# Kernel tuning notes

Hardware: AMD Instinct MI355X
Metric: run time of the kernel (lower is better)

The kernel has to match this reference:

```python
import jax, jax.numpy as jnp
import numpy as np

L = 10      # LSTM layers
H = 128     # hidden size
ENC = 4096  # traffic_encoder_output_len
B = 8192    # batch
T = 12      # points_to_predict
NUM_MODES = 25


def setup_inputs() -> dict:
    key = jax.random.key(0)
    ks = jax.random.split(key, 10)
    s = 1.0 / np.sqrt(H)
    return {
        "backbone_encoded": jax.random.normal(ks[0], (B, ENC), jnp.float32),
        "fc_in_W": jax.random.normal(ks[1], (H, ENC), jnp.float32) / np.sqrt(ENC),
        "fc_in_b": jax.random.normal(ks[2], (H,), jnp.float32) * s,
        "Wih": jax.random.normal(ks[3], (L, 4 * H, H), jnp.float32) * s,
        "Whh": jax.random.normal(ks[4], (L, 4 * H, H), jnp.float32) * s,
        "bih": jax.random.normal(ks[5], (L, 4 * H), jnp.float32) * s,
        "bhh": jax.random.normal(ks[6], (L, 4 * H), jnp.float32) * s,
        "fc_out_W": jax.random.normal(ks[7], (3 * NUM_MODES, H), jnp.float32) * s,
        "fc_out_b": jax.random.normal(ks[8], (3 * NUM_MODES,), jnp.float32) * s,
        "points_to_predict": T,
    }


def _lstm_stack(x, Wih, Whh, bih, bhh):
    # x: [B, T, H]; PyTorch gate order: i, f, g, o
    def run_layer(x, l):
        def step(carry, xt):
            h, c = carry
            gates = xt @ Wih[l].T + h @ Whh[l].T + bih[l] + bhh[l]  # [B, 4H]
            i, f, g, o = jnp.split(gates, 4, axis=-1)
            c = jax.nn.sigmoid(f) * c + jax.nn.sigmoid(i) * jnp.tanh(g)
            h = jax.nn.sigmoid(o) * jnp.tanh(c)
            return (h, c), h
        b = x.shape[0]
        h0 = jnp.zeros((b, H), x.dtype)
        _, ys = jax.lax.scan(step, (h0, h0), jnp.swapaxes(x, 0, 1))  # [T, B, H]
        return jnp.swapaxes(ys, 0, 1)

    for l in range(L):
        x = run_layer(x, l)
    return x


def reference(backbone_encoded, fc_in_W, fc_in_b, Wih, Whh, bih, bhh,
              fc_out_W, fc_out_b, points_to_predict):
    enc = jax.nn.relu(backbone_encoded @ fc_in_W.T + fc_in_b)        # [B, H]
    x = jnp.repeat(enc[:, None, :], points_to_predict, axis=1)      # [B, T, H]
    y = _lstm_stack(x, Wih, Whh, bih, bhh)                           # [B, T, H]
    fc = y @ fc_out_W.T + fc_out_b                                   # [B, T, 75]
    b, t, _ = fc.shape
    # chunk(25, dim=channels) of consecutive pairs -> [B, 25, T, 2]
    predictions = fc[:, :, :50].reshape(b, t, NUM_MODES, 2).transpose(0, 2, 1, 3)
    probabilities = jax.nn.softmax(fc[:, -1, 50:], axis=-1)          # [B, 25]
    return predictions, probabilities
```

## Files before the change

kernel.cpp:

```cpp
#include <hip/hip_runtime.h>

typedef _Float16 h16;
typedef _Float16 h4 __attribute__((ext_vector_type(4)));
typedef _Float16 h8 __attribute__((ext_vector_type(8)));
typedef float f4 __attribute__((ext_vector_type(4)));

#define NB 8192
#define NENC 4096
#define NH 128
#define NL 10
#define NT 12
#define PAD 136

#define OFF_FCIN 0
#define SZ_FCIN (128*4096)
#define OFF_W (OFF_FCIN + SZ_FCIN)
#define SZ_W (10*2*512*128)
#define OFF_FCOUT (OFF_W + SZ_W)
#define SZ_FCOUT (80*128)
#define OFF_ENC (OFF_FCOUT + SZ_FCOUT)
#define SZ_ENC (8192*128)
#define OFF_GX0 (OFF_ENC + SZ_ENC)
#define SZ_GX0 (8192*512)
#define BYTE_BIAS ((OFF_GX0 + SZ_GX0)*2)

__device__ __forceinline__ float sigf(float x) {
  float e = __builtin_amdgcn_exp2f(-1.4426950408889634f * x);
  return __builtin_amdgcn_rcpf(1.0f + e);
}
__device__ __forceinline__ float tanhf_(float x) {
  float e = __builtin_amdgcn_exp2f(-2.8853900817779268f * x);
  return 2.0f * __builtin_amdgcn_rcpf(1.0f + e) - 1.0f;
}
__device__ __forceinline__ f4 splat4(float v) { f4 r; r[0]=v; r[1]=v; r[2]=v; r[3]=v; return r; }
__device__ __forceinline__ h8 cvt8(float4 a, float4 b) {
  h8 r; r[0]=(h16)a.x; r[1]=(h16)a.y; r[2]=(h16)a.z; r[3]=(h16)a.w;
  r[4]=(h16)b.x; r[5]=(h16)b.y; r[6]=(h16)b.z; r[7]=(h16)b.w; return r;
}

__global__ __launch_bounds__(256) void prep(const float* __restrict__ fcinW,
                                            const float* __restrict__ Wih,
                                            const float* __restrict__ Whh,
                                            const float* __restrict__ bih,
                                            const float* __restrict__ bhh,
                                            const float* __restrict__ fcoutW,
                                            h16* __restrict__ wsh,
                                            float* __restrict__ wbias) {
  int idx = blockIdx.x * 256 + threadIdx.x;
  if (idx < 65536) {
    int r = idx >> 9, k8 = idx & 511;
    const float* src = fcinW + r * 4096 + k8 * 8;
    h8 v = cvt8(*(const float4*)src, *(const float4*)(src + 4));
    *(h8*)(wsh + OFF_FCIN + (((r >> 4) * 512 + k8) * 128 + (r & 15) * 8)) = v;
  } else if (idx < 229376) {
    int rel = idx - 65536;
    int l = rel >> 14, rr = rel & 16383;
    int ssel = rr >> 13, rk8 = rr & 8191;
    int r = rk8 >> 4, k8 = rk8 & 15;
    const float* src = (ssel ? Whh : Wih) + l * 65536 + r * 128 + k8 * 8;
    h8 v = cvt8(*(const float4*)src, *(const float4*)(src + 4));
    *(h8*)(wsh + OFF_W + (l * 2 + ssel) * 65536 +
           (((r >> 4) * 16 + k8) * 128 + (r & 15) * 8)) = v;
  } else if (idx < 230656) {
    int rel = idx - 229376;
    int r = rel >> 4, k8 = rel & 15;
    h8 v;
    if (r < 75) {
      const float* src = fcoutW + r * 128 + k8 * 8;
      v = cvt8(*(const float4*)src, *(const float4*)(src + 4));
    } else {
      for (int j = 0; j < 8; ++j) v[j] = (h16)0.f;
    }
    *(h8*)(wsh + OFF_FCOUT + (((r >> 4) * 16 + k8) * 128 + (r & 15) * 8)) = v;
  } else if (idx < 235776) {
    int rel = idx - 230656;
    wbias[rel] = bih[rel] + bhh[rel];
  }
}

__global__ __launch_bounds__(256) void kin(const float* __restrict__ A,
                                           const float* __restrict__ bvec,
                                           h16* __restrict__ wsh) {
  const h16* Wp = wsh + OFF_FCIN;
  h16* ench = wsh + OFF_ENC;
  int tid = threadIdx.x;
  int w = tid >> 6, lane = tid & 63, s = lane & 15, q = lane >> 4;
  int m0 = blockIdx.x * 16;
  int c0 = w * 32 + s, c1 = c0 + 16;
  f4 acc0 = splat4(bvec[c0]);
  f4 acc1 = splat4(bvec[c1]);
  const float* arow = A + (size_t)(m0 + s) * NENC;
  const h16* wp0 = Wp + (w * 2 + 0) * (512 * 128) + s * 8;
  const h16* wp1 = Wp + (w * 2 + 1) * (512 * 128) + s * 8;
#pragma unroll 4
  for (int kb = 0; kb < 128; ++kb) {
    int k0 = kb * 32 + q * 8;
    float4 x0 = *(const float4*)(arow + k0);
    float4 x1 = *(const float4*)(arow + k0 + 4);
    h8 af = cvt8(x0, x1);
    h8 b0 = *(const h8*)(wp0 + (kb * 4 + q) * 128);
    h8 b1 = *(const h8*)(wp1 + (kb * 4 + q) * 128);
    acc0 = __builtin_amdgcn_mfma_f32_16x16x32_f16(af, b0, acc0, 0, 0, 0);
    acc1 = __builtin_amdgcn_mfma_f32_16x16x32_f16(af, b1, acc1, 0, 0, 0);
  }
#pragma unroll
  for (int r = 0; r < 4; ++r) {
    int b = m0 + q * 4 + r;
    float v0 = acc0[r]; v0 = v0 > 0.f ? v0 : 0.f;
    float v1 = acc1[r]; v1 = v1 > 0.f ? v1 : 0.f;
    ench[(size_t)b * NH + c0] = (h16)v0;
    ench[(size_t)b * NH + c1] = (h16)v1;
  }
}

__global__ __launch_bounds__(256) void kin2(h16* __restrict__ wsh,
                                            const float* __restrict__ wbias) {
  int tid = threadIdx.x;
  int w2 = tid >> 6, lane = tid & 63, s = lane & 15, q = lane >> 4;
  int bid = blockIdx.x;
  int lb = bid >> 3, mt = (bid >> 2) & 1, cg = bid & 3;
  const h16* ench = wsh + OFF_ENC;
  const h16* wih0 = wsh + OFF_W;
  h16* gx0 = wsh + OFF_GX0;
  const h16* arow = ench + (size_t)(lb * 32 + mt * 16 + s) * NH;
  h8 ax[4];
#pragma unroll
  for (int kt = 0; kt < 4; ++kt) ax[kt] = *(const h8*)(arow + kt * 32 + q * 8);
#pragma unroll
  for (int ti = 0; ti < 2; ++ti) {
    int W = w2 * 2 + ti;
    int rb = cg * 8 + W;
    f4 acc = splat4(wbias[cg * 128 + W * 16 + s]);
#pragma unroll
    for (int kt = 0; kt < 4; ++kt) {
      h8 b = *(const h8*)(wih0 + (rb * 16 + kt * 4 + q) * 128 + s * 8);
      acc = __builtin_amdgcn_mfma_f32_16x16x32_f16(ax[kt], b, acc, 0, 0, 0);
    }
    h4 st; st[0] = (h16)acc[0]; st[1] = (h16)acc[1]; st[2] = (h16)acc[2]; st[3] = (h16)acc[3];
    *(h4*)(gx0 + ((((size_t)lb * 8 + W) * 8 + cg * 2 + mt) * 64 + lane) * 4) = st;
  }
}

__global__ __launch_bounds__(512, 2) void lstm(h16* __restrict__ wsh,
                                               const float* __restrict__ wbias,
                                               const float* __restrict__ fcoutb,
                                               float* __restrict__ out) {
  __shared__ h16 ring[13][32][PAD];
  __shared__ float probst[32 * 26];
  int tid = threadIdx.x;
  int w = tid >> 6, lane = tid & 63, s = lane & 15, q = lane >> 4;
  int brow = blockIdx.x * 32;
  h8 wx[4][4], wh[4][4];
  float bb[4];
  float c[2][4];

  {
    const h16* whh = wsh + OFF_W + 65536;
#pragma unroll
    for (int g = 0; g < 4; ++g)
#pragma unroll
      for (int kt = 0; kt < 4; ++kt)
        wh[g][kt] = *(const h8*)(whh + (((g * 8 + w) * 16 + kt * 4 + q) * 128) + s * 8);
    f4 gx[4][2];
    const h16* gxp = wsh + OFF_GX0 + ((size_t)blockIdx.x * 8 + w) * 8 * 256 + (size_t)lane * 4;
#pragma unroll
    for (int g = 0; g < 4; ++g)
#pragma unroll
      for (int mt = 0; mt < 2; ++mt) {
        h4 v = *(const h4*)(gxp + (g * 2 + mt) * 256);
        f4 a; a[0] = (float)v[0]; a[1] = (float)v[1]; a[2] = (float)v[2]; a[3] = (float)v[3];
        gx[g][mt] = a;
      }
#pragma unroll
    for (int mt = 0; mt < 2; ++mt)
#pragma unroll
      for (int r = 0; r < 4; ++r) c[mt][r] = 0.f;
    for (int t = 0; t < NT; ++t) {
      __syncthreads();
      int rw = t + 11; if (rw >= 13) rw -= 13;
      int rh = t + 10; if (rh >= 13) rh -= 13;
      f4 acc[4][2];
#pragma unroll
      for (int g = 0; g < 4; ++g)
#pragma unroll
        for (int mt = 0; mt < 2; ++mt) acc[g][mt] = gx[g][mt];
      if (t > 0) {
#pragma unroll
        for (int mt = 0; mt < 2; ++mt) {
          h8 ah[4];
#pragma unroll
          for (int kt = 0; kt < 4; ++kt)
            ah[kt] = *(const h8*)&ring[rh][mt * 16 + s][kt * 32 + q * 8];
#pragma unroll
          for (int g = 0; g < 4; ++g)
#pragma unroll
            for (int kt = 0; kt < 4; ++kt)
              acc[g][mt] = __builtin_amdgcn_mfma_f32_16x16x32_f16(ah[kt], wh[g][kt], acc[g][mt], 0, 0, 0);
        }
      }
#pragma unroll
      for (int mt = 0; mt < 2; ++mt)
#pragma unroll
        for (int r = 0; r < 4; ++r) {
          float iv = acc[0][mt][r], fv = acc[1][mt][r];
          float gv = acc[2][mt][r], ov = acc[3][mt][r];
          float cc = sigf(fv) * c[mt][r] + sigf(iv) * tanhf_(gv);
          c[mt][r] = cc;
          ring[rw][mt * 16 + q * 4 + r][w * 16 + s] = (h16)(sigf(ov) * tanhf_(cc));
        }
    }
  }
  for (int l = 1; l < NL; ++l) {
    const h16* wih = wsh + OFF_W + (size_t)(l * 2) * 65536;
    const h16* whh = wih + 65536;
#pragma unroll
    for (int g = 0; g < 4; ++g) {
#pragma unroll
      for (int kt = 0; kt < 4; ++kt) {
        int off = (((g * 8 + w) * 16 + kt * 4 + q) * 128) + s * 8;
        wx[g][kt] = *(const h8*)(wih + off);
        wh[g][kt] = *(const h8*)(whh + off);
      }
      bb[g] = wbias[l * 512 + g * 128 + w * 16 + s];
    }
#pragma unroll
    for (int mt = 0; mt < 2; ++mt)
#pragma unroll
      for (int r = 0; r < 4; ++r) c[mt][r] = 0.f;
    int base = 12 - l;
    for (int t = 0; t < NT; ++t) {
      __syncthreads();
      int rr = t + base; if (rr >= 13) rr -= 13;
      int rw = rr - 1; if (rw < 0) rw += 13;
      int rh = rw - 1; if (rh < 0) rh += 13;
      f4 acc[4][2];
#pragma unroll
      for (int g = 0; g < 4; ++g)
#pragma unroll
        for (int mt = 0; mt < 2; ++mt) acc[g][mt] = splat4(bb[g]);
#pragma unroll
      for (int mt = 0; mt < 2; ++mt) {
        h8 ax[4];
#pragma unroll
        for (int kt = 0; kt < 4; ++kt)
          ax[kt] = *(const h8*)&ring[rr][mt * 16 + s][kt * 32 + q * 8];
#pragma unroll
        for (int g = 0; g < 4; ++g)
#pragma unroll
          for (int kt = 0; kt < 4; ++kt)
            acc[g][mt] = __builtin_amdgcn_mfma_f32_16x16x32_f16(ax[kt], wx[g][kt], acc[g][mt], 0, 0, 0);
      }
      if (t > 0) {
#pragma unroll
        for (int mt = 0; mt < 2; ++mt) {
          h8 ah[4];
#pragma unroll
          for (int kt = 0; kt < 4; ++kt)
            ah[kt] = *(const h8*)&ring[rh][mt * 16 + s][kt * 32 + q * 8];
#pragma unroll
          for (int g = 0; g < 4; ++g)
#pragma unroll
            for (int kt = 0; kt < 4; ++kt)
              acc[g][mt] = __builtin_amdgcn_mfma_f32_16x16x32_f16(ah[kt], wh[g][kt], acc[g][mt], 0, 0, 0);
        }
      }
#pragma unroll
      for (int mt = 0; mt < 2; ++mt)
#pragma unroll
        for (int r = 0; r < 4; ++r) {
          float iv = acc[0][mt][r], fv = acc[1][mt][r];
          float gv = acc[2][mt][r], ov = acc[3][mt][r];
          float cc = sigf(fv) * c[mt][r] + sigf(iv) * tanhf_(gv);
          c[mt][r] = cc;
          ring[rw][mt * 16 + q * 4 + r][w * 16 + s] = (h16)(sigf(ov) * tanhf_(cc));
        }
    }
  }
  __syncthreads();
  h8 wo[5][4];
  float bo[5];
  const h16* fco = wsh + OFF_FCOUT;
#pragma unroll
  for (int nt = 0; nt < 5; ++nt) {
#pragma unroll
    for (int kt = 0; kt < 4; ++kt)
      wo[nt][kt] = *(const h8*)(fco + (nt * 16 + kt * 4 + q) * 128 + s * 8);
    int col = nt * 16 + s;
    bo[nt] = (col < 75) ? fcoutb[col] : 0.f;
  }
  int tcount = (w < 4) ? 2 : 1;
  for (int ti = 0; ti < tcount; ++ti) {
    int t = w + ti * 8;
    int sl = t + 2; if (sl >= 13) sl -= 13;
#pragma unroll
    for (int mt = 0; mt < 2; ++mt) {
      h8 ax[4];
#pragma unroll
      for (int kt = 0; kt < 4; ++kt)
        ax[kt] = *(const h8*)&ring[sl][mt * 16 + s][kt * 32 + q * 8];
#pragma unroll
      for (int nt = 0; nt < 5; ++nt) {
        f4 a = splat4(bo[nt]);
#pragma unroll
        for (int kt = 0; kt < 4; ++kt)
          a = __builtin_amdgcn_mfma_f32_16x16x32_f16(ax[kt], wo[nt][kt], a, 0, 0, 0);
        int col = nt * 16 + s;
#pragma unroll
        for (int r = 0; r < 4; ++r) {
          int row = mt * 16 + q * 4 + r;
          int b = brow + row;
          float v = a[r];
          if (col < 50)
            out[(size_t)b * 600 + (col >> 1) * 24 + t * 2 + (col & 1)] = v;
          if (t == 11 && col >= 50 && col < 75)
            probst[row * 26 + (col - 50)] = v;
        }
      }
    }
  }
  __syncthreads();
  if (tid < 32) {
    float vals[25];
    float m = -1e30f;
#pragma unroll
    for (int j = 0; j < 25; ++j) { vals[j] = probst[tid * 26 + j]; m = vals[j] > m ? vals[j] : m; }
    float sum = 0.f;
#pragma unroll
    for (int j = 0; j < 25; ++j) {
      float e = __builtin_amdgcn_exp2f((vals[j] - m) * 1.4426950408889634f);
      vals[j] = e; sum += e;
    }
    float rs = 1.0f / sum;
    size_t pb = (size_t)4915200 + (size_t)(brow + tid) * 25;
#pragma unroll
    for (int j = 0; j < 25; ++j) out[pb + j] = vals[j] * rs;
  }
}

extern "C" void kernel_launch(void* const* d_in, const int* in_sizes, int n_in,
                              void* d_out, int out_size, void* d_ws, size_t ws_size,
                              hipStream_t stream) {
  const float* backbone = (const float*)d_in[0];
  const float* fcinW    = (const float*)d_in[1];
  const float* fcinb    = (const float*)d_in[2];
  const float* Wih      = (const float*)d_in[3];
  const float* Whh      = (const float*)d_in[4];
  const float* bih      = (const float*)d_in[5];
  const float* bhh      = (const float*)d_in[6];
  const float* fcoutW   = (const float*)d_in[7];
  const float* fcoutb   = (const float*)d_in[8];
  h16* wsh = (h16*)d_ws;
  float* wbias = (float*)((char*)d_ws + BYTE_BIAS);

  prep<<<922, 256, 0, stream>>>(fcinW, Wih, Whh, bih, bhh, fcoutW, wsh, wbias);
  kin<<<512, 256, 0, stream>>>(backbone, fcinb, wsh);
  kin2<<<2048, 256, 0, stream>>>(wsh, wbias);
  lstm<<<256, 512, 0, stream>>>(wsh, wbias, fcoutb, (float*)d_out);
}
```

Baseline: 504.1 us.

## Software-pipeline next-step input MFMAs with gate math and merge LSTM transcendentals

Folds the four sigmoid/tanh evaluations of the LSTM cell into a shared-reciprocal form that needs two rcp calls instead of five. In layers 1+, the input-projection MFMAs for timestep t+1 are issued right after the gate math for step t, reading the next ring slot early. This lets MFMA work overlap with the transcendental VALU work and shortens the serial per-step chain. The risks are higher register pressure from carrying accumulators across steps, and possible overflow or precision loss in the product-of-denominators form.

```diff
diff --git a/kernel.cpp b/kernel.cpp
--- a/kernel.cpp
+++ b/kernel.cpp
@@ -24,18 +24,25 @@
 #define SZ_GX0 (8192*512)
 #define BYTE_BIAS ((OFF_GX0 + SZ_GX0)*2)
 
-__device__ __forceinline__ float sigf(float x) {
-  float e = __builtin_amdgcn_exp2f(-1.4426950408889634f * x);
-  return __builtin_amdgcn_rcpf(1.0f + e);
-}
-__device__ __forceinline__ float tanhf_(float x) {
-  float e = __builtin_amdgcn_exp2f(-2.8853900817779268f * x);
-  return 2.0f * __builtin_amdgcn_rcpf(1.0f + e) - 1.0f;
-}
 __device__ __forceinline__ f4 splat4(float v) { f4 r; r[0]=v; r[1]=v; r[2]=v; r[3]=v; return r; }
 __device__ __forceinline__ h8 cvt8(float4 a, float4 b) {
   h8 r; r[0]=(h16)a.x; r[1]=(h16)a.y; r[2]=(h16)a.z; r[3]=(h16)a.w;
   r[4]=(h16)b.x; r[5]=(h16)b.y; r[6]=(h16)b.z; r[7]=(h16)b.w; return r;
+}
+
+__device__ __forceinline__ h16 cell(float iv, float fv, float gv, float ov, float& c) {
+  float ei = __builtin_amdgcn_exp2f(-1.4426950408889634f * iv);
+  float ef = __builtin_amdgcn_exp2f(-1.4426950408889634f * fv);
+  float eg = __builtin_amdgcn_exp2f(-2.8853900817779268f * gv);
+  float eo = __builtin_amdgcn_exp2f(-1.4426950408889634f * ov);
+  float ai = 1.f + ei, af = 1.f + ef, ag = 1.f + eg;
+  float m1 = ai * ag;
+  float R1 = __builtin_amdgcn_rcpf(af * m1);
+  float cc = R1 * fmaf(af, 1.f - eg, c * m1);
+  c = cc;
+  float ec = __builtin_amdgcn_exp2f(-2.8853900817779268f * cc);
+  float R2 = __builtin_amdgcn_rcpf((1.f + eo) * (1.f + ec));
+  return (h16)(R2 * (1.f - ec));
 }
 
 __global__ __launch_bounds__(256) void prep(const float* __restrict__ fcinW,
@@ -202,11 +209,8 @@
       for (int mt = 0; mt < 2; ++mt)
 #pragma unroll
         for (int r = 0; r < 4; ++r) {
-          float iv = acc[0][mt][r], fv = acc[1][mt][r];
-          float gv = acc[2][mt][r], ov = acc[3][mt][r];
-          float cc = sigf(fv) * c[mt][r] + sigf(iv) * tanhf_(gv);
-          c[mt][r] = cc;
-          ring[rw][mt * 16 + q * 4 + r][w * 16 + s] = (h16)(sigf(ov) * tanhf_(cc));
+          h16 hv = cell(acc[0][mt][r], acc[1][mt][r], acc[2][mt][r], acc[3][mt][r], c[mt][r]);
+          ring[rw][mt * 16 + q * 4 + r][w * 16 + s] = hv;
         }
     }
   }
@@ -223,34 +227,34 @@
       }
       bb[g] = wbias[l * 512 + g * 128 + w * 16 + s];
     }
+    f4 acc[4][2];
+#pragma unroll
+    for (int g = 0; g < 4; ++g)
+#pragma unroll
+      for (int mt = 0; mt < 2; ++mt) acc[g][mt] = splat4(bb[g]);
 #pragma unroll
     for (int mt = 0; mt < 2; ++mt)
 #pragma unroll
       for (int r = 0; r < 4; ++r) c[mt][r] = 0.f;
-    int base = 12 - l;
     for (int t = 0; t < NT; ++t) {
       __syncthreads();
-      int rr = t + base; if (rr >= 13) rr -= 13;
-      int rw = rr - 1; if (rw < 0) rw += 13;
-      int rh = rw - 1; if (rh < 0) rh += 13;
-      f4 acc[4][2];
-#pragma unroll
-      for (int g = 0; g < 4; ++g)
-#pragma unroll
-        for (int mt = 0; mt < 2; ++mt) acc[g][mt] = splat4(bb[g]);
-#pragma unroll
-      for (int mt = 0; mt < 2; ++mt) {
-        h8 ax[4];
-#pragma unroll
-        for (int kt = 0; kt < 4; ++kt)
-          ax[kt] = *(const h8*)&ring[rr][mt * 16 + s][kt * 32 + q * 8];
-#pragma unroll
-        for (int g = 0; g < 4; ++g)
+      int rw = t + 11 - l; if (rw >= 13) rw -= 13;
+      if (t == 0) {
+        int rr = rw + 1; if (rr >= 13) rr -= 13;
+#pragma unroll
+        for (int mt = 0; mt < 2; ++mt) {
+          h8 ax[4];
 #pragma unroll
           for (int kt = 0; kt < 4; ++kt)
-            acc[g][mt] = __builtin_amdgcn_mfma_f32_16x16x32_f16(ax[kt], wx[g][kt], acc[g][mt], 0, 0, 0);
-      }
-      if (t > 0) {
+            ax[kt] = *(const h8*)&ring[rr][mt * 16 + s][kt * 32 + q * 8];
+#pragma unroll
+          for (int g = 0; g < 4; ++g)
+#pragma unroll
+            for (int kt = 0; kt < 4; ++kt)
+              acc[g][mt] = __builtin_amdgcn_mfma_f32_16x16x32_f16(ax[kt], wx[g][kt], acc[g][mt], 0, 0, 0);
+        }
+      } else {
+        int rh = rw - 1; if (rh < 0) rh += 13;
 #pragma unroll
         for (int mt = 0; mt < 2; ++mt) {
           h8 ah[4];
@@ -264,16 +268,28 @@
               acc[g][mt] = __builtin_amdgcn_mfma_f32_16x16x32_f16(ah[kt], wh[g][kt], acc[g][mt], 0, 0, 0);
         }
       }
-#pragma unroll
-      for (int mt = 0; mt < 2; ++mt)
-#pragma unroll
-        for (int r = 0; r < 4; ++r) {
-          float iv = acc[0][mt][r], fv = acc[1][mt][r];
-          float gv = acc[2][mt][r], ov = acc[3][mt][r];
-          float cc = sigf(fv) * c[mt][r] + sigf(iv) * tanhf_(gv);
-          c[mt][r] = cc;
-          ring[rw][mt * 16 + q * 4 + r][w * 16 + s] = (h16)(sigf(ov) * tanhf_(cc));
-        }
+      int rx = rw + 2; if (rx >= 13) rx -= 13;
+#pragma unroll
+      for (int mt = 0; mt < 2; ++mt) {
+        h8 axn[4];
+#pragma unroll
+        for (int kt = 0; kt < 4; ++kt)
+          axn[kt] = *(const h8*)&ring[rx][mt * 16 + s][kt * 32 + q * 8];
+        h16 hv[4];
+#pragma unroll
+        for (int r = 0; r < 4; ++r)
+          hv[r] = cell(acc[0][mt][r], acc[1][mt][r], acc[2][mt][r], acc[3][mt][r], c[mt][r]);
+#pragma unroll
+        for (int g = 0; g < 4; ++g) acc[g][mt] = splat4(bb[g]);
+#pragma unroll
+        for (int g = 0; g < 4; ++g)
+#pragma unroll
+          for (int kt = 0; kt < 4; ++kt)
+            acc[g][mt] = __builtin_amdgcn_mfma_f32_16x16x32_f16(axn[kt], wx[g][kt], acc[g][mt], 0, 0, 0);
+#pragma unroll
+        for (int r = 0; r < 4; ++r)
+          ring[rw][mt * 16 + q * 4 + r][w * 16 + s] = hv[r];
+      }
     }
   }
   __syncthreads();
```

Measured after the change: 498.7 us. About the same (-1.1%).
